# Optimization experiments

Hardware: AMD Instinct MI355X
Metric: run time of the kernel (lower is better)

## Reference

```python
import jax, jax.numpy as jnp
import numpy as np

N = 50000
E = 800000
D_IN = 1000
D_H2 = 128  # h_dim * multiple
D_H = 16


def gat_conv(x, src, dst, W, attn_l, attn_r, bias, n):
    """DGL-style GATConv (no dropout, no activation). Returns [n, H, F]."""
    H, F = attn_l.shape
    feat = (x @ W).reshape(n, H, F)                      # [N,H,F]
    el = jnp.sum(feat * attn_l[None], axis=-1)           # [N,H]
    er = jnp.sum(feat * attn_r[None], axis=-1)           # [N,H]
    e = jax.nn.leaky_relu(el[src] + er[dst], 0.2)        # [E,H]
    emax = jax.ops.segment_max(e, dst, num_segments=n)   # [N,H] per-dst softmax max
    ee = jnp.exp(e - emax[dst])                          # [E,H]
    denom = jax.ops.segment_sum(ee, dst, num_segments=n) # [N,H]
    alpha = ee / denom[dst]                              # [E,H]
    msg = feat[src] * alpha[..., None]                   # [E,H,F]
    out = jax.ops.segment_sum(msg, dst, num_segments=n)  # [N,H,F]
    return out + bias.reshape(1, H, F)


def setup_inputs() -> dict:
    key = jax.random.key(0)
    ks = jax.random.split(key, 24)
    rn = lambda k, shp, s=0.05: (jax.random.normal(k, shp, dtype=jnp.float32) * s)
    inp = {
        "x": rn(ks[0], (N, D_IN), 1.0),
        "src": jax.random.randint(ks[1], (E,), 0, N, dtype=jnp.int32),
        "dst": jax.random.randint(ks[2], (E,), 0, N, dtype=jnp.int32),
        "W1": rn(ks[3], (D_IN, D_H2)),
        "al1": rn(ks[4], (1, D_H2)),
        "ar1": rn(ks[5], (1, D_H2)),
        "b1": jnp.zeros((D_H2,), jnp.float32),
        "W2": rn(ks[6], (D_H2, 2 * D_H2)),
        "al2": rn(ks[7], (2, D_H2)),
        "ar2": rn(ks[8], (2, D_H2)),
        "b2": jnp.zeros((2 * D_H2,), jnp.float32),
        "Wm": rn(ks[9], (D_H2, 2 * D_H)),
        "alm": rn(ks[10], (2, D_H)),
        "arm": rn(ks[11], (2, D_H)),
        "bm": jnp.zeros((2 * D_H,), jnp.float32),
        "Wv": rn(ks[12], (D_H2, 2 * D_H)),
        "alv": rn(ks[13], (2, D_H)),
        "arv": rn(ks[14], (2, D_H)),
        "bv": jnp.zeros((2 * D_H,), jnp.float32),
        "eps": rn(ks[15], (N, D_H), 1.0),
    }
    return inp


def reference(x, src, dst, W1, al1, ar1, b1, W2, al2, ar2, b2,
              Wm, alm, arm, bm, Wv, alv, arv, bv, eps):
    n = x.shape[0]
    o = gat_conv(x, src, dst, W1, al1, ar1, b1, n).mean(-2)           # [N,128]
    o = gat_conv(o, src, dst, W2, al2, ar2, b2, n).mean(-2) + o       # residual
    mean = gat_conv(o, src, dst, Wm, alm, arm, bm, n).mean(-2)        # [N,16]
    var = jnp.exp(gat_conv(o, src, dst, Wv, alv, arv, bv, n).mean(-2))
    z = mean + jnp.sqrt(var) * eps                                    # reparameterize
    return z, mean, var
```

## Files before the change

### kernel.cpp

```cpp
#include <hip/hip_runtime.h>
#include <hip/hip_bf16.h>
#include <math.h>

typedef unsigned short u16;
typedef unsigned int u32;
typedef __attribute__((ext_vector_type(8))) __bf16 bf16x8;
typedef __attribute__((ext_vector_type(4))) float f32x4;
typedef __attribute__((ext_vector_type(4))) u32 u32x4;
typedef __attribute__((ext_vector_type(2))) u32 u32x2;

#define NNODES 50000
#define NEDGES 800000

__device__ __forceinline__ float bf2f(u16 u) {
    union { u32 i; float f; } v; v.i = ((u32)u) << 16; return v.f;
}
__device__ __forceinline__ u16 f2bf(float x) {
    union { float f; u32 i; } v; v.f = x;
    u32 r = v.i + 0x7fffu + ((v.i >> 16) & 1u);
    return (u16)(r >> 16);
}
__device__ __forceinline__ float lrelu(float x) { return x >= 0.f ? x : 0.2f * x; }

__device__ __forceinline__ void gload_lds16(const u16* g, u16* l) {
    __builtin_amdgcn_global_load_lds((const __attribute__((address_space(1))) u32*)g,
                                     (__attribute__((address_space(3))) u32*)l, 16, 0, 0);
}

__global__ __launch_bounds__(256) void k_zero2(int* a, int* b, int count) {
    int i = blockIdx.x * 256 + threadIdx.x;
    if (i < count) { a[i] = 0; b[i] = 0; }
}

__global__ __launch_bounds__(256) void k_count(const int* __restrict__ dst, int* __restrict__ counts, int e) {
    int i = blockIdx.x * 256 + threadIdx.x;
    if (i < e) atomicAdd(&counts[dst[i]], 1);
}

__global__ __launch_bounds__(256) void k_scan1(const int* __restrict__ counts, int* __restrict__ row_ptr,
                                               int* __restrict__ bsums, int n) {
    __shared__ int tmp[256];
    int t = threadIdx.x, i = blockIdx.x * 256 + t;
    int v = (i < n) ? counts[i] : 0;
    tmp[t] = v; __syncthreads();
    for (int off = 1; off < 256; off <<= 1) {
        int x = 0; if (t >= off) x = tmp[t - off];
        __syncthreads(); tmp[t] += x; __syncthreads();
    }
    if (i < n) row_ptr[i] = tmp[t] - v;
    if (t == 255) bsums[blockIdx.x] = tmp[255];
}

__global__ __launch_bounds__(256) void k_scan2(int* bsums, int nb) {
    __shared__ int tmp[256];
    int t = threadIdx.x;
    int v = (t < nb) ? bsums[t] : 0;
    tmp[t] = v; __syncthreads();
    for (int off = 1; off < 256; off <<= 1) {
        int x = 0; if (t >= off) x = tmp[t - off];
        __syncthreads(); tmp[t] += x; __syncthreads();
    }
    if (t < nb) bsums[t] = tmp[t] - v;
}

__global__ __launch_bounds__(256) void k_scan3(int* __restrict__ row_ptr, const int* __restrict__ bsums,
                                               int n, int total) {
    int i = blockIdx.x * 256 + threadIdx.x;
    if (i < n) row_ptr[i] += bsums[blockIdx.x];
    if (i == 0) row_ptr[n] = total;
}

__global__ __launch_bounds__(256) void k_fill(const int* __restrict__ src, const int* __restrict__ dst,
                                              const int* __restrict__ row_ptr, int* __restrict__ cursor,
                                              int* __restrict__ esrc, int e) {
    int i = blockIdx.x * 256 + threadIdx.x;
    if (i < e) {
        int d = dst[i];
        int p = row_ptr[d] + atomicAdd(&cursor[d], 1);
        esrc[p] = src[i];
    }
}

__global__ __launch_bounds__(256) void k_prep(const float* __restrict__ W1, const float* __restrict__ W2,
                                              const float* __restrict__ Wm, const float* __restrict__ Wv,
                                              const float* __restrict__ al2, const float* __restrict__ ar2,
                                              const float* __restrict__ b2,
                                              u16* __restrict__ W1t, u16* __restrict__ Wct,
                                              u16* __restrict__ Bmvt,
                                              float* __restrict__ ul, float* __restrict__ ur,
                                              float* __restrict__ bmean) {
    int b = blockIdx.x, t = threadIdx.x;
    if (b < 500) {
        int i = b * 256 + t;
        int k = i >> 7, n = i & 127;
        W1t[(size_t)n * 1000 + k] = f2bf(W1[i]);
    } else if (b < 628) {
        int i = (b - 500) * 256 + t;
        int f = i >> 8, c = i & 255, h = c >> 7, k = c & 127;
        Wct[i] = f2bf(0.5f * W2[(size_t)k * 256 + h * 128 + f]);
    } else if (b == 628) {
        int h = t >> 7, k = t & 127;
        const float* wrow = W2 + (size_t)k * 256 + h * 128;
        const float* alh = al2 + h * 128;
        const float* arh = ar2 + h * 128;
        float sl = 0.f, sr = 0.f;
        for (int f = 0; f < 128; f += 4) {
            f32x4 w = *(const f32x4*)(wrow + f);
            f32x4 a = *(const f32x4*)(alh + f);
            f32x4 r = *(const f32x4*)(arh + f);
#pragma unroll
            for (int q = 0; q < 4; q++) { sl += w[q] * a[q]; sr += w[q] * r[q]; }
        }
        ul[t] = sl; ur[t] = sr;
        if (t < 128) bmean[t] = 0.5f * (b2[t] + b2[128 + t]);
    } else {
        for (int i = t; i < 64 * 128; i += 256) {
            int c = i >> 7, k = i & 127;
            Bmvt[i] = f2bf(c < 32 ? Wm[(size_t)k * 32 + c] : Wv[(size_t)k * 32 + (c - 32)]);
        }
    }
}

__device__ __forceinline__ void load_af(const float* __restrict__ arow, int k0, int K, bf16x8& a) {
    if (k0 + 8 <= K) {
        f32x4 a0 = *(const f32x4*)(arow + k0);
        f32x4 a1 = *(const f32x4*)(arow + k0 + 4);
#pragma unroll
        for (int j = 0; j < 4; j++) { a[j] = (__bf16)a0[j]; a[4 + j] = (__bf16)a1[j]; }
    } else {
#pragma unroll
        for (int j = 0; j < 8; j++) a[j] = (__bf16)0.f;
    }
}
__device__ __forceinline__ void load_af(const u16* __restrict__ arow, int k0, int K, bf16x8& a) {
    if (k0 + 8 <= K) a = *(const bf16x8*)(arow + k0);
    else {
#pragma unroll
        for (int j = 0; j < 8; j++) a[j] = (__bf16)0.f;
    }
}

template <typename AT, int MODE>
__global__ __launch_bounds__(256) void k_gemm_tiled(const AT* __restrict__ A, const u16* __restrict__ Bt,
                                                    u16* __restrict__ C, int M, int Nn, int K,
                                                    const float* __restrict__ bias,
                                                    const u16* __restrict__ resid,
                                                    const float* __restrict__ al,
                                                    const float* __restrict__ ar,
                                                    float* __restrict__ el, float* __restrict__ er) {
    __shared__ __align__(16) u16 lb[32 * 128 * 8];
    const int tid = threadIdx.x;
    const int wave = tid >> 6, lane = tid & 63;
    const int m = lane & 15, quad = lane >> 4;
    const int row0 = blockIdx.x * 64 + wave * 16;

    f32x4 acc[8];
#pragma unroll
    for (int t = 0; t < 8; t++)
#pragma unroll
        for (int r = 0; r < 4; r++) acc[t][r] = 0.f;

    int arr = row0 + m; if (arr > M - 1) arr = M - 1;
    const AT* arow = A + (size_t)arr * K;
    const int scol = tid & 127, shi = tid >> 7;
    const u16* bcol = Bt + (size_t)scol * K;
    u16* sdst = &lb[((size_t)shi * 128 + scol) * 8];

    const int KC = 256;
    const int nchunks = (K + KC - 1) / KC;
    bf16x8 afr[8];

    for (int c = 0; c < nchunks; ++c) {
        const int kb = c * KC;
#pragma unroll
        for (int ks = 0; ks < 8; ++ks)
            load_af(arow, kb + ks * 32 + quad * 8, K, afr[ks]);
#pragma unroll
        for (int it = 0; it < 16; ++it) {
            int kq = kb + (it * 2 + shi) * 8;
            if (kq < K) gload_lds16(bcol + kq, sdst + it * 2048);
        }
        __syncthreads();
#pragma unroll
        for (int ks = 0; ks < 8; ++ks) {
#pragma unroll
            for (int t = 0; t < 8; ++t) {
                bf16x8 b = *(const bf16x8*)&lb[((ks * 4 + quad) * 128 + t * 16 + m) * 8];
                acc[t] = __builtin_amdgcn_mfma_f32_16x16x32_bf16(afr[ks], b, acc[t], 0, 0, 0);
            }
        }
        __syncthreads();
    }

#pragma unroll
    for (int r = 0; r < 4; r++) {
        int row = row0 + quad * 4 + r;
        if (MODE == 0) {
            float pe = 0.f, pr = 0.f;
#pragma unroll
            for (int t = 0; t < 8; t++) {
                float a = acc[t][r];
                int c = t * 16 + m;
                pe += a * al[c]; pr += a * ar[c];
            }
#pragma unroll
            for (int off = 8; off; off >>= 1) { pe += __shfl_xor(pe, off); pr += __shfl_xor(pr, off); }
            if (m == 0 && row < M) { el[row] = pe; er[row] = pr; }
        }
#pragma unroll
        for (int t = 0; t < 8; t++) {
            int col = t * 16 + m;
            if (row < M) {
                float v = acc[t][r];
                if (MODE == 1) v += bias[col] + bf2f(resid[(size_t)row * Nn + col]);
                C[(size_t)row * Nn + col] = f2bf(v);
            }
        }
    }
}

__global__ __launch_bounds__(64) void k_gemmmv(const u16* __restrict__ A, const u16* __restrict__ Bt,
                                               u16* __restrict__ featmv,
                                               const float* __restrict__ alm, const float* __restrict__ arm,
                                               const float* __restrict__ alv, const float* __restrict__ arv,
                                               float* __restrict__ elm, float* __restrict__ erm,
                                               float* __restrict__ elv, float* __restrict__ erv, int M) {
    int row0 = blockIdx.x * 16;
    int lane = threadIdx.x;
    int m = lane & 15, quad = lane >> 4;
    f32x4 acc[4];
#pragma unroll
    for (int t = 0; t < 4; t++)
#pragma unroll
        for (int r = 0; r < 4; r++) acc[t][r] = 0.f;

    const u16* arow = A + (size_t)(row0 + m) * 128 + quad * 8;
#pragma unroll
    for (int s = 0; s < 4; ++s) {
        bf16x8 a = *(const bf16x8*)(arow + s * 32);
#pragma unroll
        for (int t = 0; t < 4; t++) {
            bf16x8 b = *(const bf16x8*)(Bt + (size_t)(t * 16 + m) * 128 + s * 32 + quad * 8);
            acc[t] = __builtin_amdgcn_mfma_f32_16x16x32_bf16(a, b, acc[t], 0, 0, 0);
        }
    }
#pragma unroll
    for (int r = 0; r < 4; r++) {
        int row = row0 + quad * 4 + r;
#pragma unroll
        for (int t = 0; t < 4; t++) {
            float a = acc[t][r];
            const float* alp = (t < 2) ? alm : alv;
            const float* arp = (t < 2) ? arm : arv;
            float pe = a * alp[(t & 1) * 16 + m];
            float pr = a * arp[(t & 1) * 16 + m];
#pragma unroll
            for (int off = 8; off; off >>= 1) { pe += __shfl_xor(pe, off); pr += __shfl_xor(pr, off); }
            if (m == 0 && row < M) {
                float* elp = (t < 2) ? elm : elv;
                float* erp = (t < 2) ? erm : erv;
                elp[row * 2 + (t & 1)] = pe; erp[row * 2 + (t & 1)] = pr;
            }
            if (row < M) featmv[(size_t)row * 64 + t * 16 + m] = f2bf(a);
        }
    }
}

__global__ __launch_bounds__(256) void k_agg1(const int* __restrict__ row_ptr, const int* __restrict__ esrc,
                                              const u16* __restrict__ feat, const float* __restrict__ el,
                                              const float* __restrict__ er, const float* __restrict__ bias,
                                              const float* __restrict__ ul, const float* __restrict__ ur,
                                              u16* __restrict__ o_bf, float* __restrict__ el2,
                                              float* __restrict__ er2, int n) {
    int wave = threadIdx.x >> 6, lane = threadIdx.x & 63;
    int l = lane & 31;
    int node = blockIdx.x * 8 + wave * 2 + (lane >> 5);
    if (node >= n) node = n - 1;
    int beg = row_ptr[node], deg = row_ptr[node + 1] - beg;
    float erd = er[node];
    int degmax = max(deg, __shfl_xor(deg, 32));
    const int srcb = lane & 32;
    float acc0 = 0.f, acc1 = 0.f, acc2 = 0.f, acc3 = 0.f, den = 0.f;
    for (int off0 = 0; off0 < degmax; off0 += 32) {
        float w = 0.f; int s = 0;
        if (off0 + l < deg) { s = esrc[beg + off0 + l]; w = expf(lrelu(el[s] + erd)); }
        den += w;
        int cnt = min(32, degmax - off0);
        int j = 0;
        for (; j + 4 <= cnt; j += 4) {
            int s0 = __shfl(s, srcb + j),     s1 = __shfl(s, srcb + j + 1);
            int s2 = __shfl(s, srcb + j + 2), s3 = __shfl(s, srcb + j + 3);
            float w0 = __shfl(w, srcb + j),     w1 = __shfl(w, srcb + j + 1);
            float w2 = __shfl(w, srcb + j + 2), w3 = __shfl(w, srcb + j + 3);
            u32x2 p0 = ((const u32x2*)(feat + (size_t)s0 * 128))[l];
            u32x2 p1 = ((const u32x2*)(feat + (size_t)s1 * 128))[l];
            u32x2 p2 = ((const u32x2*)(feat + (size_t)s2 * 128))[l];
            u32x2 p3 = ((const u32x2*)(feat + (size_t)s3 * 128))[l];
            acc0 += w0 * bf2f((u16)(p0.x & 0xffff)) + w1 * bf2f((u16)(p1.x & 0xffff))
                  + w2 * bf2f((u16)(p2.x & 0xffff)) + w3 * bf2f((u16)(p3.x & 0xffff));
            acc1 += w0 * bf2f((u16)(p0.x >> 16)) + w1 * bf2f((u16)(p1.x >> 16))
                  + w2 * bf2f((u16)(p2.x >> 16)) + w3 * bf2f((u16)(p3.x >> 16));
            acc2 += w0 * bf2f((u16)(p0.y & 0xffff)) + w1 * bf2f((u16)(p1.y & 0xffff))
                  + w2 * bf2f((u16)(p2.y & 0xffff)) + w3 * bf2f((u16)(p3.y & 0xffff));
            acc3 += w0 * bf2f((u16)(p0.y >> 16)) + w1 * bf2f((u16)(p1.y >> 16))
                  + w2 * bf2f((u16)(p2.y >> 16)) + w3 * bf2f((u16)(p3.y >> 16));
        }
        for (; j < cnt; ++j) {
            int sj = __shfl(s, srcb + j);
            float wj = __shfl(w, srcb + j);
            u32x2 pv = ((const u32x2*)(feat + (size_t)sj * 128))[l];
            acc0 += wj * bf2f((u16)(pv.x & 0xffff));
            acc1 += wj * bf2f((u16)(pv.x >> 16));
            acc2 += wj * bf2f((u16)(pv.y & 0xffff));
            acc3 += wj * bf2f((u16)(pv.y >> 16));
        }
    }
#pragma unroll
    for (int off = 16; off; off >>= 1) den += __shfl_xor(den, off);
    float inv = (den > 0.f) ? 1.f / den : 0.f;
    const int c0 = 4 * l;
    float o0 = acc0 * inv + bias[c0];
    float o1 = acc1 * inv + bias[c0 + 1];
    float o2 = acc2 * inv + bias[c0 + 2];
    float o3 = acc3 * inv + bias[c0 + 3];
#pragma unroll
    for (int h = 0; h < 2; ++h) {
        const float* ulh = ul + h * 128 + c0;
        const float* urh = ur + h * 128 + c0;
        float pe = o0 * ulh[0] + o1 * ulh[1] + o2 * ulh[2] + o3 * ulh[3];
        float pr = o0 * urh[0] + o1 * urh[1] + o2 * urh[2] + o3 * urh[3];
#pragma unroll
        for (int off = 16; off; off >>= 1) { pe += __shfl_xor(pe, off); pr += __shfl_xor(pr, off); }
        if (l == 0) { el2[node * 2 + h] = pe; er2[node * 2 + h] = pr; }
    }
    u32x2 pv;
    pv.x = (u32)f2bf(o0) | ((u32)f2bf(o1) << 16);
    pv.y = (u32)f2bf(o2) | ((u32)f2bf(o3) << 16);
    ((u32x2*)(o_bf + (size_t)node * 128))[l] = pv;
}

__global__ __launch_bounds__(256) void k_agg2o(const int* __restrict__ row_ptr, const int* __restrict__ esrc,
                                               const u16* __restrict__ o_in, const float* __restrict__ el,
                                               const float* __restrict__ er, u16* __restrict__ agg, int n) {
    int wave = threadIdx.x >> 6, lane = threadIdx.x & 63;
    int l = lane & 31;
    int node = blockIdx.x * 8 + wave * 2 + (lane >> 5);
    if (node >= n) node = n - 1;
    int beg = row_ptr[node], deg = row_ptr[node + 1] - beg;
    float er0 = er[node * 2], er1 = er[node * 2 + 1];
    int degmax = max(deg, __shfl_xor(deg, 32));
    const int srcb = lane & 32;
    float a00 = 0.f, a01 = 0.f, a02 = 0.f, a03 = 0.f;
    float a10 = 0.f, a11 = 0.f, a12 = 0.f, a13 = 0.f;
    float d0 = 0.f, d1 = 0.f;
    for (int off0 = 0; off0 < degmax; off0 += 32) {
        float w0 = 0.f, w1 = 0.f; int s = 0;
        if (off0 + l < deg) {
            s = esrc[beg + off0 + l];
            float2 e2 = *(const float2*)(el + 2 * s);
            w0 = expf(lrelu(e2.x + er0));
            w1 = expf(lrelu(e2.y + er1));
        }
        d0 += w0; d1 += w1;
        int cnt = min(32, degmax - off0);
        int j = 0;
        for (; j + 4 <= cnt; j += 4) {
            int sa = __shfl(s, srcb + j),     sb = __shfl(s, srcb + j + 1);
            int sc = __shfl(s, srcb + j + 2), sd = __shfl(s, srcb + j + 3);
            float w0a = __shfl(w0, srcb + j),     w0b = __shfl(w0, srcb + j + 1);
            float w0c = __shfl(w0, srcb + j + 2), w0d = __shfl(w0, srcb + j + 3);
            float w1a = __shfl(w1, srcb + j),     w1b = __shfl(w1, srcb + j + 1);
            float w1c = __shfl(w1, srcb + j + 2), w1d = __shfl(w1, srcb + j + 3);
            u32x2 pa = ((const u32x2*)(o_in + (size_t)sa * 128))[l];
            u32x2 pb = ((const u32x2*)(o_in + (size_t)sb * 128))[l];
            u32x2 pc = ((const u32x2*)(o_in + (size_t)sc * 128))[l];
            u32x2 pd = ((const u32x2*)(o_in + (size_t)sd * 128))[l];
            float fa0 = bf2f((u16)(pa.x & 0xffff)), fa1 = bf2f((u16)(pa.x >> 16));
            float fa2 = bf2f((u16)(pa.y & 0xffff)), fa3 = bf2f((u16)(pa.y >> 16));
            float fb0 = bf2f((u16)(pb.x & 0xffff)), fb1 = bf2f((u16)(pb.x >> 16));
            float fb2 = bf2f((u16)(pb.y & 0xffff)), fb3 = bf2f((u16)(pb.y >> 16));
            float fc0 = bf2f((u16)(pc.x & 0xffff)), fc1 = bf2f((u16)(pc.x >> 16));
            float fc2 = bf2f((u16)(pc.y & 0xffff)), fc3 = bf2f((u16)(pc.y >> 16));
            float fd0 = bf2f((u16)(pd.x & 0xffff)), fd1 = bf2f((u16)(pd.x >> 16));
            float fd2 = bf2f((u16)(pd.y & 0xffff)), fd3 = bf2f((u16)(pd.y >> 16));
            a00 += w0a * fa0 + w0b * fb0 + w0c * fc0 + w0d * fd0;
            a01 += w0a * fa1 + w0b * fb1 + w0c * fc1 + w0d * fd1;
            a02 += w0a * fa2 + w0b * fb2 + w0c * fc2 + w0d * fd2;
            a03 += w0a * fa3 + w0b * fb3 + w0c * fc3 + w0d * fd3;
            a10 += w1a * fa0 + w1b * fb0 + w1c * fc0 + w1d * fd0;
            a11 += w1a * fa1 + w1b * fb1 + w1c * fc1 + w1d * fd1;
            a12 += w1a * fa2 + w1b * fb2 + w1c * fc2 + w1d * fd2;
            a13 += w1a * fa3 + w1b * fb3 + w1c * fc3 + w1d * fd3;
        }
        for (; j < cnt; ++j) {
            int sj = __shfl(s, srcb + j);
            float w0j = __shfl(w0, srcb + j), w1j = __shfl(w1, srcb + j);
            u32x2 pv = ((const u32x2*)(o_in + (size_t)sj * 128))[l];
            float f0 = bf2f((u16)(pv.x & 0xffff)), f1 = bf2f((u16)(pv.x >> 16));
            float f2 = bf2f((u16)(pv.y & 0xffff)), f3 = bf2f((u16)(pv.y >> 16));
            a00 += w0j * f0; a01 += w0j * f1; a02 += w0j * f2; a03 += w0j * f3;
            a10 += w1j * f0; a11 += w1j * f1; a12 += w1j * f2; a13 += w1j * f3;
        }
    }
#pragma unroll
    for (int off = 16; off; off >>= 1) { d0 += __shfl_xor(d0, off); d1 += __shfl_xor(d1, off); }
    float i0 = (d0 > 0.f) ? 1.f / d0 : 0.f, i1 = (d1 > 0.f) ? 1.f / d1 : 0.f;
    u32x2 p0, p1;
    p0.x = (u32)f2bf(a00 * i0) | ((u32)f2bf(a01 * i0) << 16);
    p0.y = (u32)f2bf(a02 * i0) | ((u32)f2bf(a03 * i0) << 16);
    p1.x = (u32)f2bf(a10 * i1) | ((u32)f2bf(a11 * i1) << 16);
    p1.y = (u32)f2bf(a12 * i1) | ((u32)f2bf(a13 * i1) << 16);
    u32x2* aw = (u32x2*)(agg + (size_t)node * 256);
    aw[l] = p0;
    aw[32 + l] = p1;
}

__global__ __launch_bounds__(256) void k_aggmv(const int* __restrict__ row_ptr, const int* __restrict__ esrc,
                                               const u16* __restrict__ featmv,
                                               const float* __restrict__ elm, const float* __restrict__ erm,
                                               const float* __restrict__ elv, const float* __restrict__ erv,
                                               const float* __restrict__ bm, const float* __restrict__ bv,
                                               const float* __restrict__ eps, float* __restrict__ out, int n) {
    __shared__ float wsm[256 * 4];
    __shared__ int ssm[256];
    int tid = threadIdx.x;
    int wave = tid >> 6, lane = tid & 63;
    int l = lane & 31;
    int node = blockIdx.x * 8 + wave * 2 + (lane >> 5);
    if (node >= n) node = n - 1;
    int tbl = l >> 4, h = (l >> 3) & 1;
    const int wtype = l >> 3;
    int beg = row_ptr[node], deg = row_ptr[node + 1] - beg;
    float erm0 = erm[2 * node], erm1 = erm[2 * node + 1];
    float erv0 = erv[2 * node], erv1 = erv[2 * node + 1];
    int degmax = max(deg, __shfl_xor(deg, 32));
    const int bidx = wave * 64 + (lane & 32);
    float acc0 = 0.f, acc1 = 0.f;
    float dm0 = 0.f, dm1 = 0.f, dv0 = 0.f, dv1 = 0.f;
    for (int off0 = 0; off0 < degmax; off0 += 32) {
        float wm0 = 0.f, wm1 = 0.f, wv0 = 0.f, wv1 = 0.f; int s = 0;
        if (off0 + l < deg) {
            s = esrc[beg + off0 + l];
            float2 em = *(const float2*)(elm + 2 * s);
            float2 ev = *(const float2*)(elv + 2 * s);
            wm0 = expf(lrelu(em.x + erm0));
            wm1 = expf(lrelu(em.y + erm1));
            wv0 = expf(lrelu(ev.x + erv0));
            wv1 = expf(lrelu(ev.y + erv1));
        }
        dm0 += wm0; dm1 += wm1; dv0 += wv0; dv1 += wv1;
        f32x4 wq; wq[0] = wm0; wq[1] = wm1; wq[2] = wv0; wq[3] = wv1;
        *(f32x4*)&wsm[tid * 4] = wq;
        ssm[tid] = s;
        int cnt = min(32, degmax - off0);
        int j = 0;
        for (; j + 2 <= cnt; j += 2) {
            int sa = ssm[bidx + j], sb = ssm[bidx + j + 1];
            float wa = wsm[(bidx + j) * 4 + wtype];
            float wb = wsm[(bidx + j + 1) * 4 + wtype];
            u32 pa = ((const u32*)(featmv + (size_t)sa * 64))[l];
            u32 pb = ((const u32*)(featmv + (size_t)sb * 64))[l];
            acc0 += wa * bf2f((u16)(pa & 0xffff)) + wb * bf2f((u16)(pb & 0xffff));
            acc1 += wa * bf2f((u16)(pa >> 16)) + wb * bf2f((u16)(pb >> 16));
        }
        for (; j < cnt; ++j) {
            int sj = ssm[bidx + j];
            float wj = wsm[(bidx + j) * 4 + wtype];
            u32 pv = ((const u32*)(featmv + (size_t)sj * 64))[l];
            acc0 += wj * bf2f((u16)(pv & 0xffff));
            acc1 += wj * bf2f((u16)(pv >> 16));
        }
    }
#pragma unroll
    for (int off = 16; off; off >>= 1) {
        dm0 += __shfl_xor(dm0, off); dm1 += __shfl_xor(dm1, off);
        dv0 += __shfl_xor(dv0, off); dv1 += __shfl_xor(dv1, off);
    }
    float den = tbl ? (h ? dv1 : dv0) : (h ? dm1 : dm0);
    float inv = (den > 0.f) ? 1.f / den : 0.f;
    const int fidx0 = (2 * l) & 31;
    float bias0 = tbl ? bv[fidx0] : bm[fidx0];
    float bias1 = tbl ? bv[fidx0 + 1] : bm[fidx0 + 1];
    float outc0 = acc0 * inv + bias0;
    float outc1 = acc1 * inv + bias1;
    float hm0 = 0.5f * (outc0 + __shfl_xor(outc0, 8));
    float hm1 = 0.5f * (outc1 + __shfl_xor(outc1, 8));
    int srcv = (lane & 32) + 16 + (l & 7);
    float vp0 = __shfl(hm0, srcv);
    float vp1 = __shfl(hm1, srcv);
    if (l < 8) {
        int f0 = 2 * l;
        float var0 = expf(vp0), var1 = expf(vp1);
        float2 e2 = *(const float2*)(eps + (size_t)node * 16 + f0);
        float z0 = hm0 + sqrtf(var0) * e2.x;
        float z1 = hm1 + sqrtf(var1) * e2.y;
        size_t base = (size_t)node * 16 + f0;
        *(float2*)(out + base) = make_float2(z0, z1);
        *(float2*)(out + (size_t)NNODES * 16 + base) = make_float2(hm0, hm1);
        *(float2*)(out + (size_t)2 * NNODES * 16 + base) = make_float2(var0, var1);
    }
}

extern "C" void kernel_launch(void* const* d_in, const int* in_sizes, int n_in,
                              void* d_out, int out_size, void* d_ws, size_t ws_size,
                              hipStream_t stream) {
    const int N = NNODES, E = NEDGES;
    const float* x   = (const float*)d_in[0];
    const int* src   = (const int*)d_in[1];
    const int* dst   = (const int*)d_in[2];
    const float* W1  = (const float*)d_in[3];
    const float* al1 = (const float*)d_in[4];
    const float* ar1 = (const float*)d_in[5];
    const float* b1  = (const float*)d_in[6];
    const float* W2  = (const float*)d_in[7];
    const float* al2 = (const float*)d_in[8];
    const float* ar2 = (const float*)d_in[9];
    const float* b2  = (const float*)d_in[10];
    const float* Wm  = (const float*)d_in[11];
    const float* alm = (const float*)d_in[12];
    const float* arm = (const float*)d_in[13];
    const float* bm  = (const float*)d_in[14];
    const float* Wv  = (const float*)d_in[15];
    const float* alv = (const float*)d_in[16];
    const float* arv = (const float*)d_in[17];
    const float* bv  = (const float*)d_in[18];
    const float* eps = (const float*)d_in[19];
    float* out = (float*)d_out;

    char* ws = (char*)d_ws;
    size_t off = 0;
    auto take = [&](size_t bytes) { size_t r = off; off += (bytes + 255) & ~(size_t)255; return r; };
    int* counts   = (int*)(ws + take((size_t)N * 4));
    int* cursor   = (int*)(ws + take((size_t)N * 4));
    int* row_ptr  = (int*)(ws + take((size_t)(N + 1) * 4));
    int* bsums    = (int*)(ws + take(256 * 4));
    int* esrc     = (int*)(ws + take((size_t)E * 4));
    u16* W1t      = (u16*)(ws + take((size_t)128 * 1000 * 2));
    u16* Wct      = (u16*)(ws + take((size_t)128 * 256 * 2));
    u16* Bmvt     = (u16*)(ws + take((size_t)64 * 128 * 2));
    float* ul2    = (float*)(ws + take(256 * 4));
    float* ur2    = (float*)(ws + take(256 * 4));
    float* bmean  = (float*)(ws + take(128 * 4));
    float* el1    = (float*)(ws + take((size_t)N * 4));
    float* er1    = (float*)(ws + take((size_t)N * 4));
    float* el2    = (float*)(ws + take((size_t)N * 2 * 4));
    float* er2    = (float*)(ws + take((size_t)N * 2 * 4));
    float* elm    = (float*)(ws + take((size_t)N * 2 * 4));
    float* erm    = (float*)(ws + take((size_t)N * 2 * 4));
    float* elv    = (float*)(ws + take((size_t)N * 2 * 4));
    float* erv    = (float*)(ws + take((size_t)N * 2 * 4));
    u16* o_bf     = (u16*)(ws + take((size_t)N * 128 * 2));
    u16* o2_bf    = (u16*)(ws + take((size_t)N * 128 * 2));
    u16* R        = (u16*)(ws + take((size_t)N * 256 * 2));
    u16* feat1    = R;
    u16* agg      = R;
    u16* featmv   = R;
    (void)ws_size; (void)n_in; (void)in_sizes; (void)out_size;

    const int nb = (N + 255) / 256;
    const int eb = (E + 255) / 256;
    const int wb8 = (N + 7) / 8;
    const int gb = (N + 63) / 64;

    k_prep<<<dim3(630), 256, 0, stream>>>(W1, W2, Wm, Wv, al2, ar2, b2, W1t, Wct, Bmvt, ul2, ur2, bmean);

    k_zero2<<<dim3(nb), 256, 0, stream>>>(counts, cursor, N);
    k_count<<<dim3(eb), 256, 0, stream>>>(dst, counts, E);
    k_scan1<<<dim3(nb), 256, 0, stream>>>(counts, row_ptr, bsums, N);
    k_scan2<<<dim3(1), 256, 0, stream>>>(bsums, nb);
    k_scan3<<<dim3(nb), 256, 0, stream>>>(row_ptr, bsums, N, E);
    k_fill<<<dim3(eb), 256, 0, stream>>>(src, dst, row_ptr, cursor, esrc, E);

    k_gemm_tiled<float, 0><<<dim3(gb), 256, 0, stream>>>(x, W1t, feat1, N, 128, 1000,
                                                         nullptr, nullptr, al1, ar1, el1, er1);
    k_agg1<<<dim3(wb8), 256, 0, stream>>>(row_ptr, esrc, feat1, el1, er1, b1, ul2, ur2,
                                          o_bf, el2, er2, N);

    k_agg2o<<<dim3(wb8), 256, 0, stream>>>(row_ptr, esrc, o_bf, el2, er2, agg, N);
    k_gemm_tiled<u16, 1><<<dim3(gb), 256, 0, stream>>>(agg, Wct, o2_bf, N, 128, 256,
                                                       bmean, o_bf, nullptr, nullptr, nullptr, nullptr);

    k_gemmmv<<<dim3(N / 16), 64, 0, stream>>>(o2_bf, Bmvt, featmv, alm, arm, alv, arv,
                                              elm, erm, elv, erv, N);
    k_aggmv<<<dim3(wb8), 256, 0, stream>>>(row_ptr, esrc, featmv, elm, erm, elv, erv,
                                           bm, bv, eps, out, N);
}
```

Before: 579.2 us.

## Stage A tile through LDS with coalesced loads and register prefetch of next chunk

The GEMM kernel now loads the A operand cooperatively in coalesced row segments, converts it to bf16 and stores it in a padded LDS tile, instead of each lane gathering strided 8-element fragments directly from global memory. The next K-chunk's A data is prefetched into registers while the current chunk's MFMAs run. The K chunk shrinks from 256 to 128 to fit the extra A buffer. This aims to improve coalescing of the large fp32 x read and hide global latency, at the cost of more barriers per K and an extra LDS round trip.

```diff
diff --git a/kernel.cpp b/kernel.cpp
--- a/kernel.cpp
+++ b/kernel.cpp
@@ -121,25 +121,6 @@
     }
 }
 
-__device__ __forceinline__ void load_af(const float* __restrict__ arow, int k0, int K, bf16x8& a) {
-    if (k0 + 8 <= K) {
-        f32x4 a0 = *(const f32x4*)(arow + k0);
-        f32x4 a1 = *(const f32x4*)(arow + k0 + 4);
-#pragma unroll
-        for (int j = 0; j < 4; j++) { a[j] = (__bf16)a0[j]; a[4 + j] = (__bf16)a1[j]; }
-    } else {
-#pragma unroll
-        for (int j = 0; j < 8; j++) a[j] = (__bf16)0.f;
-    }
-}
-__device__ __forceinline__ void load_af(const u16* __restrict__ arow, int k0, int K, bf16x8& a) {
-    if (k0 + 8 <= K) a = *(const bf16x8*)(arow + k0);
-    else {
-#pragma unroll
-        for (int j = 0; j < 8; j++) a[j] = (__bf16)0.f;
-    }
-}
-
 template <typename AT, int MODE>
 __global__ __launch_bounds__(256) void k_gemm_tiled(const AT* __restrict__ A, const u16* __restrict__ Bt,
                                                     u16* __restrict__ C, int M, int Nn, int K,
@@ -148,11 +129,13 @@
                                                     const float* __restrict__ al,
                                                     const float* __restrict__ ar,
                                                     float* __restrict__ el, float* __restrict__ er) {
-    __shared__ __align__(16) u16 lb[32 * 128 * 8];
+    __shared__ __align__(16) u16 Alds[64 * 136];
+    __shared__ __align__(16) u16 Blds[16 * 128 * 8];
     const int tid = threadIdx.x;
     const int wave = tid >> 6, lane = tid & 63;
     const int m = lane & 15, quad = lane >> 4;
-    const int row0 = blockIdx.x * 64 + wave * 16;
+    const int row0b = blockIdx.x * 64;
+    const int row0 = row0b + wave * 16;
 
     f32x4 acc[8];
 #pragma unroll
@@ -160,34 +143,90 @@
 #pragma unroll
         for (int r = 0; r < 4; r++) acc[t][r] = 0.f;
 
-    int arr = row0 + m; if (arr > M - 1) arr = M - 1;
-    const AT* arow = A + (size_t)arr * K;
     const int scol = tid & 127, shi = tid >> 7;
     const u16* bcol = Bt + (size_t)scol * K;
-    u16* sdst = &lb[((size_t)shi * 128 + scol) * 8];
-
-    const int KC = 256;
+
+    const int KC = 128;
     const int nchunks = (K + KC - 1) / KC;
-    bf16x8 afr[8];
+
+    f32x4 aregf[8];
+    u32x4 aregh[4];
+
+    auto issueA = [&](int kb) {
+        if constexpr (sizeof(AT) == 4) {
+#pragma unroll
+            for (int i = 0; i < 8; ++i) {
+                int u = i * 256 + tid;
+                int rw = u >> 5, sg = u & 31;
+                int arr = row0b + rw; if (arr > M - 1) arr = M - 1;
+                int k0 = kb + sg * 4;
+                f32x4 v = {0.f, 0.f, 0.f, 0.f};
+                if (k0 + 4 <= K) v = *(const f32x4*)((const float*)A + (size_t)arr * K + k0);
+                aregf[i] = v;
+            }
+        } else {
+#pragma unroll
+            for (int i = 0; i < 4; ++i) {
+                int u = i * 256 + tid;
+                int rw = u >> 4, sg = u & 15;
+                int arr = row0b + rw; if (arr > M - 1) arr = M - 1;
+                int k0 = kb + sg * 8;
+                u32x4 v = {0, 0, 0, 0};
+                if (k0 + 8 <= K) v = *(const u32x4*)((const u16*)A + (size_t)arr * K + k0);
+                aregh[i] = v;
+            }
+        }
+    };
+    auto writeA = [&]() {
+        if constexpr (sizeof(AT) == 4) {
+#pragma unroll
+            for (int i = 0; i < 8; ++i) {
+                int u = i * 256 + tid;
+                int rw = u >> 5, sg = u & 31;
+                u32x2 pk;
+                pk.x = ((u32)f2bf(aregf[i][1]) << 16) | f2bf(aregf[i][0]);
+                pk.y = ((u32)f2bf(aregf[i][3]) << 16) | f2bf(aregf[i][2]);
+                *(u32x2*)&Alds[rw * 136 + sg * 4] = pk;
+            }
+        } else {
+#pragma unroll
+            for (int i = 0; i < 4; ++i) {
+                int u = i * 256 + tid;
+                int rw = u >> 4, sg = u & 15;
+                *(u32x4*)&Alds[rw * 136 + sg * 8] = aregh[i];
+            }
+        }
+    };
+    auto stageB = [&](int kb) {
+#pragma unroll
+        for (int it = 0; it < 8; ++it) {
+            int g = it * 2 + shi;
+            int kq = kb + g * 8;
+            if (kq < K) gload_lds16(bcol + kq, &Blds[((size_t)g * 128 + scol) * 8]);
+        }
+    };
+
+    issueA(0);
+    writeA();
+    stageB(0);
+    __syncthreads();
 
     for (int c = 0; c < nchunks; ++c) {
-        const int kb = c * KC;
-#pragma unroll
-        for (int ks = 0; ks < 8; ++ks)
-            load_af(arow, kb + ks * 32 + quad * 8, K, afr[ks]);
-#pragma unroll
-        for (int it = 0; it < 16; ++it) {
-            int kq = kb + (it * 2 + shi) * 8;
-            if (kq < K) gload_lds16(bcol + kq, sdst + it * 2048);
+        const int kbn = (c + 1) * KC;
+        if (c + 1 < nchunks) issueA(kbn);
+#pragma unroll
+        for (int ks = 0; ks < 4; ++ks) {
+            bf16x8 a = *(const bf16x8*)&Alds[(wave * 16 + m) * 136 + ks * 32 + quad * 8];
+#pragma unroll
+            for (int t = 0; t < 8; ++t) {
+                bf16x8 b = *(const bf16x8*)&Blds[((ks * 4 + quad) * 128 + t * 16 + m) * 8];
+                acc[t] = __builtin_amdgcn_mfma_f32_16x16x32_bf16(a, b, acc[t], 0, 0, 0);
+            }
         }
         __syncthreads();
-#pragma unroll
-        for (int ks = 0; ks < 8; ++ks) {
-#pragma unroll
-            for (int t = 0; t < 8; ++t) {
-                bf16x8 b = *(const bf16x8*)&lb[((ks * 4 + quad) * 128 + t * 16 + m) * 8];
-                acc[t] = __builtin_amdgcn_mfma_f32_16x16x32_bf16(afr[ks], b, acc[t], 0, 0, 0);
-            }
+        if (c + 1 < nchunks) {
+            writeA();
+            stageB(kbn);
         }
         __syncthreads();
     }
```

Result: faster. 567.7 us (-2.0%).
